# Kernel optimization log

Hardware: AMD Instinct MI355X
Metric: run time of the kernel (lower is better)

Reference implementation:

```python
import jax, jax.numpy as jnp
import numpy as np

T, P, E, H = 200000, 100000, 600000, 256

def setup_inputs() -> dict:
    key = jax.random.key(0)
    ks = jax.random.split(key, 8)
    x = jax.random.normal(ks[0], (T, H), dtype=jnp.float32)
    points = jax.random.normal(ks[1], (P, 3), dtype=jnp.float32)
    triangles = jax.random.randint(ks[2], (T, 3), 0, P)
    triangle_edges = jax.random.randint(ks[3], (2, E), 0, T)
    din = H + 9
    W1 = jax.random.normal(ks[4], (din, H), dtype=jnp.float32) / np.sqrt(din)
    b1 = jnp.zeros((H,), dtype=jnp.float32)
    W2 = jax.random.normal(ks[5], (H, H), dtype=jnp.float32) / np.sqrt(H)
    b2 = jnp.zeros((H,), dtype=jnp.float32)
    return {"x": x, "points": points, "triangles": triangles,
            "triangle_edges": triangle_edges, "W1": W1, "b1": b1, "W2": W2, "b2": b2}

def reference(x, points, triangles, triangle_edges, W1, b1, W2, b2):
    # Per-triangle geometry: [T, 3(corners), 3(xyz)]
    tp = points[triangles]
    e_ij = tp[:, 0] - tp[:, 1]
    e_ik = tp[:, 0] - tp[:, 2]
    e_jk = tp[:, 1] - tp[:, 2]
    edge_vectors = jnp.stack([e_ij, e_ik, e_jk], axis=1)  # [T,3,3]
    t_max = jnp.max(edge_vectors, axis=1).astype(x.dtype)  # [T,3]
    t_min = jnp.min(edge_vectors, axis=1).astype(x.dtype)  # [T,3]
    barycenters = jnp.mean(tp, axis=1).astype(x.dtype)     # [T,3]

    src = triangle_edges[0]
    tgt = triangle_edges[1]
    # Relative geometric descriptor per edge: [E, 9]
    r_n_k = jnp.concatenate([t_min[src] - t_min[tgt],
                             t_max[src] - t_max[tgt],
                             barycenters[src] - barycenters[tgt]], axis=1)
    feature_diff = x[src] - x[tgt]                          # [E, H]
    mlp_in = jnp.concatenate([r_n_k, feature_diff], axis=1)  # [E, H+9]
    h = jax.nn.relu(mlp_in @ W1 + b1)
    mlp_out = h @ W2 + b2                                   # [E, H]
    # Scatter-add back to source triangles (order-independent sum)
    new_features = jax.ops.segment_sum(mlp_out, src, num_segments=x.shape[0])
    return new_features.astype(x.dtype)
```

## Files before the change

### kernel.cpp

```cpp
#include <hip/hip_runtime.h>
#include <stdint.h>

typedef float f32x4v __attribute__((ext_vector_type(4)));
typedef short short8v __attribute__((ext_vector_type(8)));

__device__ __forceinline__ float bf2f(unsigned short u) {
  union { uint32_t i; float f; } v; v.i = ((uint32_t)u) << 16; return v.f;
}
__device__ __forceinline__ unsigned short f2bf(float f) {
  union { float f; uint32_t i; } v; v.f = f;
  uint32_t x = v.i;
  uint32_t r = (x + 0x7FFFu + ((x >> 16) & 1u)) >> 16;
  return (unsigned short)r;
}
__device__ __forceinline__ short8v cvt8(float4 a, float4 b) {
  short8v v;
  v[0] = (short)f2bf(a.x); v[1] = (short)f2bf(a.y);
  v[2] = (short)f2bf(a.z); v[3] = (short)f2bf(a.w);
  v[4] = (short)f2bf(b.x); v[5] = (short)f2bf(b.y);
  v[6] = (short)f2bf(b.z); v[7] = (short)f2bf(b.w);
  return v;
}

__global__ void zero_kernel(int* __restrict__ p, int n4) {
  int i = blockIdx.x * blockDim.x + threadIdx.x;
  int stride = gridDim.x * blockDim.x;
  for (; i < n4; i += stride) ((int4*)p)[i] = make_int4(0, 0, 0, 0);
}

__global__ void setup_kernel(const float* __restrict__ W1, const float* __restrict__ W2,
                             const float* __restrict__ points, const int* __restrict__ tri,
                             const int* __restrict__ te,
                             unsigned short* __restrict__ W1fT, unsigned short* __restrict__ W2T,
                             float* __restrict__ geo12, int* __restrict__ count,
                             int T, int E) {
  int i = blockIdx.x * blockDim.x + threadIdx.x;
  if (i < 256 * 288) {
    int n = i / 288, k = i % 288;
    float v = 0.f;
    if (k < 256) v = W1[(9 + k) * 256 + n];
    else if (k < 265) v = W1[(k - 256) * 256 + n];
    W1fT[i] = f2bf(v);
  }
  if (i < 256 * 256) {
    int n = i >> 8, k = i & 255;
    W2T[i] = f2bf(W2[k * 256 + n]);
  }
  if (i < T) {
    int t = i;
    int i0 = tri[3 * t], i1 = tri[3 * t + 1], i2 = tri[3 * t + 2];
    float g[12];
#pragma unroll
    for (int c = 0; c < 3; ++c) {
      float p0 = points[i0 * 3 + c], p1 = points[i1 * 3 + c], p2 = points[i2 * 3 + c];
      float e0 = p0 - p1, e1 = p0 - p2, e2 = p1 - p2;
      float mx = fmaxf(e0, fmaxf(e1, e2));
      float mn = fminf(e0, fminf(e1, e2));
      float bc = (p0 + p1 + p2) * (1.0f / 3.0f);
      g[c] = mn; g[3 + c] = mx; g[6 + c] = bc;
    }
    g[9] = 0.f; g[10] = 0.f; g[11] = 0.f;
    float4* o = (float4*)(geo12 + (size_t)t * 12);
    o[0] = make_float4(g[0], g[1], g[2], g[3]);
    o[1] = make_float4(g[4], g[5], g[6], g[7]);
    o[2] = make_float4(g[8], g[9], g[10], g[11]);
  }
  if (i < E) atomicAdd(&count[te[i]], 1);
}

__global__ void scan1_kernel(const int* __restrict__ count, int* __restrict__ incl,
                             int* __restrict__ blocksum, int T) {
  __shared__ int wsums[4];
  int tid = threadIdx.x, wave = tid >> 6, lane = tid & 63;
  int idx0 = blockIdx.x * 1024 + tid * 4;
  int c0 = 0, c1 = 0, c2 = 0, c3 = 0;
  if (idx0 + 3 < T) {
    int4 v = *(const int4*)(count + idx0);
    c0 = v.x; c1 = v.y; c2 = v.z; c3 = v.w;
  } else {
    if (idx0 < T) c0 = count[idx0];
    if (idx0 + 1 < T) c1 = count[idx0 + 1];
    if (idx0 + 2 < T) c2 = count[idx0 + 2];
  }
  int s = c0 + c1 + c2 + c3;
  int inclv = s;
#pragma unroll
  for (int off = 1; off < 64; off <<= 1) {
    int n = __shfl_up(inclv, off);
    if (lane >= off) inclv += n;
  }
  if (lane == 63) wsums[wave] = inclv;
  __syncthreads();
  int wbase = 0;
#pragma unroll
  for (int w = 0; w < 4; ++w) if (w < wave) wbase += wsums[w];
  int base = wbase + inclv - s;
  int e0 = base + c0, e1 = e0 + c1, e2 = e1 + c2, e3 = e2 + c3;
  if (idx0 < T) incl[idx0] = e0;
  if (idx0 + 1 < T) incl[idx0 + 1] = e1;
  if (idx0 + 2 < T) incl[idx0 + 2] = e2;
  if (idx0 + 3 < T) incl[idx0 + 3] = e3;
  if (tid == 255) blocksum[blockIdx.x] = wbase + inclv;
}

__global__ void scan2_kernel(const int* __restrict__ blocksum, int* __restrict__ blockbase, int nb) {
  __shared__ int wsums[4];
  int tid = threadIdx.x, wave = tid >> 6, lane = tid & 63;
  int v = (tid < nb) ? blocksum[tid] : 0;
  int inclv = v;
#pragma unroll
  for (int off = 1; off < 64; off <<= 1) {
    int n = __shfl_up(inclv, off);
    if (lane >= off) inclv += n;
  }
  if (lane == 63) wsums[wave] = inclv;
  __syncthreads();
  int wbase = 0;
#pragma unroll
  for (int w = 0; w < 4; ++w) if (w < wave) wbase += wsums[w];
  if (tid < nb) blockbase[tid] = wbase + inclv - v;
}

__global__ void scan3_kernel(const int* __restrict__ count, const int* __restrict__ incl,
                             const int* __restrict__ blockbase, int* __restrict__ offsets,
                             int* __restrict__ cursor, int T) {
  int idx = blockIdx.x * 1024 + threadIdx.x * 4;
  int bb = blockbase[blockIdx.x];
#pragma unroll
  for (int j = 0; j < 4; ++j) {
    int i = idx + j;
    if (i < T) {
      int o = incl[i] + bb;
      offsets[i + 1] = o;
      cursor[i] = o - count[i];
    }
  }
  if (blockIdx.x == 0 && threadIdx.x == 0) offsets[0] = 0;
}

__global__ void fill_kernel(const int* __restrict__ te, int* __restrict__ cursor,
                            int* __restrict__ tgt_list, int E) {
  int e = blockIdx.x * blockDim.x + threadIdx.x;
  if (e < E) {
    int s = te[e];
    int pos = atomicAdd(&cursor[s], 1);
    tgt_list[pos] = te[E + e];
  }
}

__launch_bounds__(1024, 4)
__global__ void ugemm_kernel(const float* __restrict__ x, const float* __restrict__ geo12,
                             const unsigned short* __restrict__ W1fT,
                             unsigned short* __restrict__ U, int T) {
  __shared__ alignas(16) unsigned short Bl[73728];
  int tid = threadIdx.x;
#pragma unroll
  for (int j = 0; j < 9; ++j) {
    int idx = tid + j * 1024;
    int n = idx / 36, c = idx % 36;
    int pc = (c < 32) ? (c ^ (n & 7)) : (32 + ((c - 32) ^ (n & 3)));
    short8v v = *(const short8v*)(W1fT + (size_t)n * 288 + c * 8);
    *(short8v*)(&Bl[n * 288 + pc * 8]) = v;
  }
  __syncthreads();
  int wid = tid >> 6, lane = tid & 63;
  int l15 = lane & 15, lhi = lane >> 4;
  int r7 = l15 & 7, r3 = l15 & 3;
  const unsigned short* lane_b = &Bl[l15 * 288];
  int strip = blockIdx.x * 16 + wid;
  if (strip * 16 >= T) return;
  int row = strip * 16 + l15;
  const float* xrow = x + (size_t)row * 256 + 8 * lhi;
  float4 ga = make_float4(0, 0, 0, 0), gb = make_float4(0, 0, 0, 0);
  if (lhi < 2) {
    const float* gp = geo12 + (size_t)row * 12 + lhi * 8;
    ga = *(const float4*)gp;
    gb = *(const float4*)(gp + 4);
  }
  float4 pa[4], pb[4];
#pragma unroll
  for (int k = 0; k < 4; ++k) {
    pa[k] = *(const float4*)(xrow + k * 32);
    pb[k] = *(const float4*)(xrow + k * 32 + 4);
  }
  f32x4v acc[16] = {};
#pragma unroll
  for (int kk = 0; kk < 8; ++kk) {
    float4 ca = pa[kk & 3], cb = pb[kk & 3];
    if (kk < 4) {
      pa[kk & 3] = *(const float4*)(xrow + (kk + 4) * 32);
      pb[kk & 3] = *(const float4*)(xrow + (kk + 4) * 32 + 4);
    }
    short8v av = cvt8(ca, cb);
    int pc = (kk * 4 + lhi) ^ r7;
    const unsigned short* bptr = lane_b + pc * 8;
#pragma unroll
    for (int nf = 0; nf < 16; ++nf) {
      short8v bv = *(const short8v*)(bptr + nf * 4608);
      acc[nf] = __builtin_amdgcn_mfma_f32_16x16x32_bf16(av, bv, acc[nf], 0, 0, 0);
    }
  }
  {
    short8v av = cvt8(ga, gb);
    int pc = 32 + (lhi ^ r3);
    const unsigned short* bptr = lane_b + pc * 8;
#pragma unroll
    for (int nf = 0; nf < 16; ++nf) {
      short8v bv = *(const short8v*)(bptr + nf * 4608);
      acc[nf] = __builtin_amdgcn_mfma_f32_16x16x32_bf16(av, bv, acc[nf], 0, 0, 0);
    }
  }
#pragma unroll
  for (int i = 0; i < 4; ++i) {
    int m = strip * 16 + 4 * lhi + i;
    unsigned short* urow = U + (size_t)m * 256 + l15;
#pragma unroll
    for (int nf = 0; nf < 16; ++nf)
      urow[nf * 16] = f2bf(acc[nf][i]);
  }
}

__launch_bounds__(256, 4)
__global__ void gather_kernel(const unsigned short* __restrict__ U,
                              const int* __restrict__ offsets,
                              const int* __restrict__ tgt_list,
                              const float* __restrict__ b1,
                              unsigned short* __restrict__ sum_h, int T) {
  int gid = blockIdx.x * blockDim.x + threadIdx.x;
  int half = (T + 1) >> 1;
  int pair = gid >> 5;
  if (pair >= half) return;
  int c8 = (gid & 31) * 8;
  int tA = pair, tB = pair + half;
  bool hasRowB = tB < T;
  int begA = offsets[tA], endA = offsets[tA + 1];
  int begB = hasRowB ? offsets[tB] : 0, endB = hasRowB ? offsets[tB + 1] : 0;
  float b1r[8];
  {
    float4 a = *(const float4*)(b1 + c8);
    float4 b = *(const float4*)(b1 + c8 + 4);
    b1r[0] = a.x; b1r[1] = a.y; b1r[2] = a.z; b1r[3] = a.w;
    b1r[4] = b.x; b1r[5] = b.y; b1r[6] = b.z; b1r[7] = b.w;
  }
  short8v uva = *(const short8v*)(U + (size_t)tA * 256 + c8);
  short8v uvb = *(const short8v*)(U + (size_t)(hasRowB ? tB : tA) * 256 + c8);
  float uA[8], sA[8], uB[8], sB[8];
#pragma unroll
  for (int j = 0; j < 8; ++j) {
    uA[j] = bf2f((unsigned short)uva[j]) + b1r[j]; sA[j] = 0.f;
    uB[j] = bf2f((unsigned short)uvb[j]) + b1r[j]; sB[j] = 0.f;
  }
  int eiA = begA, eiB = begB;
  while (eiA < endA || eiB < endB) {
    bool hasA = eiA < endA, hasB = eiB < endB;
    int laA = hasA ? endA - 1 : 0;
    int laB = hasB ? endB - 1 : 0;
    int a0 = hasA ? eiA : 0;
    int a1 = hasA ? min(eiA + 1, laA) : 0;
    int a2 = hasA ? min(eiA + 2, laA) : 0;
    int a3 = hasA ? min(eiA + 3, laA) : 0;
    int b0 = hasB ? eiB : 0;
    int b1i = hasB ? min(eiB + 1, laB) : 0;
    int b2i = hasB ? min(eiB + 2, laB) : 0;
    int b3 = hasB ? min(eiB + 3, laB) : 0;
    int gA0 = tgt_list[a0], gA1 = tgt_list[a1], gA2 = tgt_list[a2], gA3 = tgt_list[a3];
    int gB0 = tgt_list[b0], gB1 = tgt_list[b1i], gB2 = tgt_list[b2i], gB3 = tgt_list[b3];
    short8v vA0 = *(const short8v*)(U + (size_t)gA0 * 256 + c8);
    short8v vA1 = *(const short8v*)(U + (size_t)gA1 * 256 + c8);
    short8v vA2 = *(const short8v*)(U + (size_t)gA2 * 256 + c8);
    short8v vA3 = *(const short8v*)(U + (size_t)gA3 * 256 + c8);
    short8v vB0 = *(const short8v*)(U + (size_t)gB0 * 256 + c8);
    short8v vB1 = *(const short8v*)(U + (size_t)gB1 * 256 + c8);
    short8v vB2 = *(const short8v*)(U + (size_t)gB2 * 256 + c8);
    short8v vB3 = *(const short8v*)(U + (size_t)gB3 * 256 + c8);
    float mA0 = hasA ? 1.f : 0.f;
    float mA1 = (hasA && eiA + 1 <= laA) ? 1.f : 0.f;
    float mA2 = (hasA && eiA + 2 <= laA) ? 1.f : 0.f;
    float mA3 = (hasA && eiA + 3 <= laA) ? 1.f : 0.f;
    float mB0 = hasB ? 1.f : 0.f;
    float mB1 = (hasB && eiB + 1 <= laB) ? 1.f : 0.f;
    float mB2 = (hasB && eiB + 2 <= laB) ? 1.f : 0.f;
    float mB3 = (hasB && eiB + 3 <= laB) ? 1.f : 0.f;
#pragma unroll
    for (int j = 0; j < 8; ++j) {
      sA[j] += mA0 * fmaxf(uA[j] - bf2f((unsigned short)vA0[j]), 0.f)
             + mA1 * fmaxf(uA[j] - bf2f((unsigned short)vA1[j]), 0.f)
             + mA2 * fmaxf(uA[j] - bf2f((unsigned short)vA2[j]), 0.f)
             + mA3 * fmaxf(uA[j] - bf2f((unsigned short)vA3[j]), 0.f);
      sB[j] += mB0 * fmaxf(uB[j] - bf2f((unsigned short)vB0[j]), 0.f)
             + mB1 * fmaxf(uB[j] - bf2f((unsigned short)vB1[j]), 0.f)
             + mB2 * fmaxf(uB[j] - bf2f((unsigned short)vB2[j]), 0.f)
             + mB3 * fmaxf(uB[j] - bf2f((unsigned short)vB3[j]), 0.f);
    }
    if (hasA) eiA += 4;
    if (hasB) eiB += 4;
  }
  short8v hva, hvb;
#pragma unroll
  for (int j = 0; j < 8; ++j) { hva[j] = (short)f2bf(sA[j]); hvb[j] = (short)f2bf(sB[j]); }
  *(short8v*)(sum_h + (size_t)tA * 256 + c8) = hva;
  if (hasRowB) *(short8v*)(sum_h + (size_t)tB * 256 + c8) = hvb;
}

__launch_bounds__(1024, 4)
__global__ void out_gemm_kernel(const unsigned short* __restrict__ sum_h,
                                const unsigned short* __restrict__ W2T,
                                const int* __restrict__ count,
                                const float* __restrict__ b2,
                                float* __restrict__ out, int T) {
  __shared__ alignas(16) unsigned short Bl[65536];
  int tid = threadIdx.x;
#pragma unroll
  for (int j = 0; j < 8; ++j) {
    int idx = tid + j * 1024;
    int n = idx >> 5, c = idx & 31;
    int pc = c ^ (n & 7);
    short8v v = *(const short8v*)(W2T + (size_t)n * 256 + c * 8);
    *(short8v*)(&Bl[n * 256 + pc * 8]) = v;
  }
  __syncthreads();
  int wid = tid >> 6, lane = tid & 63;
  int l15 = lane & 15, lhi = lane >> 4;
  int r7 = l15 & 7;
  const unsigned short* lane_b = &Bl[l15 * 256];
  int strip = blockIdx.x * 16 + wid;
  if (strip * 16 >= T) return;
  int row = strip * 16 + l15;
  const unsigned short* arow = sum_h + (size_t)row * 256 + 8 * lhi;
  short8v pa[8];
#pragma unroll
  for (int k = 0; k < 8; ++k) pa[k] = *(const short8v*)(arow + k * 32);
  float b2r[16];
#pragma unroll
  for (int nf = 0; nf < 16; ++nf) b2r[nf] = b2[nf * 16 + l15];
  f32x4v acc[16] = {};
#pragma unroll
  for (int kk = 0; kk < 8; ++kk) {
    short8v av = pa[kk];
    int pc = (kk * 4 + lhi) ^ r7;
    const unsigned short* bptr = lane_b + pc * 8;
#pragma unroll
    for (int nf = 0; nf < 16; ++nf) {
      short8v bv = *(const short8v*)(bptr + nf * 4096);
      acc[nf] = __builtin_amdgcn_mfma_f32_16x16x32_bf16(av, bv, acc[nf], 0, 0, 0);
    }
  }
#pragma unroll
  for (int i = 0; i < 4; ++i) {
    int m = strip * 16 + 4 * lhi + i;
    float cnt = (float)count[m];
    float* orow = out + (size_t)m * 256 + l15;
#pragma unroll
    for (int nf = 0; nf < 16; ++nf)
      orow[nf * 16] = acc[nf][i] + cnt * b2r[nf];
  }
}

extern "C" void kernel_launch(void* const* d_in, const int* in_sizes, int n_in,
                              void* d_out, int out_size, void* d_ws, size_t ws_size,
                              hipStream_t stream) {
  const float* x = (const float*)d_in[0];
  const float* points = (const float*)d_in[1];
  const int* triangles = (const int*)d_in[2];
  const int* te = (const int*)d_in[3];
  const float* W1 = (const float*)d_in[4];
  const float* b1 = (const float*)d_in[5];
  const float* W2 = (const float*)d_in[6];
  const float* b2 = (const float*)d_in[7];
  float* out = (float*)d_out;
  int T = in_sizes[0] / 256;
  int E = in_sizes[3] / 2;

  char* ws = (char*)d_ws;
  size_t off = 0;
  auto alloc = [&](size_t bytes) {
    void* p = ws + off;
    off = (off + bytes + 255) & ~(size_t)255;
    return p;
  };
  unsigned short* U     = (unsigned short*)alloc((size_t)T * 256 * 2);
  float*          geo12 = (float*)alloc(((size_t)T * 12 + 16) * 4);
  unsigned short* W1fT  = (unsigned short*)alloc((size_t)256 * 288 * 2);
  unsigned short* W2T   = (unsigned short*)alloc((size_t)256 * 256 * 2);
  int* count   = (int*)alloc((size_t)(T + 4) * 4);
  int* offsets = (int*)alloc((size_t)(T + 1) * 4);
  int* cursor  = (int*)alloc((size_t)T * 4);
  int* tgtl    = (int*)alloc((size_t)E * 4);
  int* incl    = (int*)alloc((size_t)T * 4);
  int* bsum    = (int*)alloc(256 * 4);
  int* bbase   = (int*)alloc(256 * 4);
  unsigned short* sum_h = (unsigned short*)alloc((size_t)T * 256 * 2);
  if (off > ws_size) return;

  int nb1 = (T + 1023) / 1024;
  int nstrips = (T + 15) / 16;
  int ngemm = (nstrips + 15) / 16;
  zero_kernel<<<200, 256, 0, stream>>>(count, (T + 3) / 4);
  {
    int mx = max(E, max(T, 256 * 288));
    setup_kernel<<<(mx + 255) / 256, 256, 0, stream>>>(W1, W2, points, triangles, te,
                                                       W1fT, W2T, geo12, count, T, E);
  }
  scan1_kernel<<<nb1, 256, 0, stream>>>(count, incl, bsum, T);
  scan2_kernel<<<1, 256, 0, stream>>>(bsum, bbase, nb1);
  scan3_kernel<<<nb1, 256, 0, stream>>>(count, incl, bbase, offsets, cursor, T);
  fill_kernel<<<(E + 255) / 256, 256, 0, stream>>>(te, cursor, tgtl, E);
  ugemm_kernel<<<ngemm, 1024, 0, stream>>>(x, geo12, W1fT, U, T);
  {
    int half = (T + 1) >> 1;
    gather_kernel<<<(half * 32 + 255) / 256, 256, 0, stream>>>(U, offsets, tgtl, b1, sum_h, T);
  }
  out_gemm_kernel<<<ngemm, 1024, 0, stream>>>(sum_h, W2T, count, b2, out, T);
}
```

Before: 331.9 us.

## Retile GEMM waves to 32x128 tiles sharing B fragments across two row blocks

Both the U GEMM and the output GEMM now give each wave 32 rows by 128 columns instead of 16 rows by 256 columns, with two waves splitting N per strip. Each B fragment read from LDS feeds two MFMAs, which halves LDS traffic per MFMA. The A prefetch depth is cut from four slots to two to hold register pressure steady. The cost is that every x/sum_h row is now loaded by two waves, doubling global reads of A, which L2 is expected to absorb.

```diff
diff --git a/kernel.cpp b/kernel.cpp
--- a/kernel.cpp
+++ b/kernel.cpp
@@ -166,57 +166,75 @@
   int wid = tid >> 6, lane = tid & 63;
   int l15 = lane & 15, lhi = lane >> 4;
   int r7 = l15 & 7, r3 = l15 & 3;
-  const unsigned short* lane_b = &Bl[l15 * 288];
-  int strip = blockIdx.x * 16 + wid;
-  if (strip * 16 >= T) return;
-  int row = strip * 16 + l15;
-  const float* xrow = x + (size_t)row * 256 + 8 * lhi;
-  float4 ga = make_float4(0, 0, 0, 0), gb = make_float4(0, 0, 0, 0);
-  if (lhi < 2) {
-    const float* gp = geo12 + (size_t)row * 12 + lhi * 8;
-    ga = *(const float4*)gp;
-    gb = *(const float4*)(gp + 4);
-  }
-  float4 pa[4], pb[4];
-#pragma unroll
-  for (int k = 0; k < 4; ++k) {
-    pa[k] = *(const float4*)(xrow + k * 32);
-    pb[k] = *(const float4*)(xrow + k * 32 + 4);
-  }
-  f32x4v acc[16] = {};
+  int strip = blockIdx.x * 8 + (wid >> 1);
+  int nhalf = wid & 1;
+  const unsigned short* lane_b = &Bl[(nhalf * 128 + l15) * 288];
+  if (strip * 32 >= T) return;
+  int row0 = strip * 32 + l15;
+  int row1 = row0 + 16;
+  const float* xr0 = x + (size_t)row0 * 256 + 8 * lhi;
+  const float* xr1 = x + (size_t)row1 * 256 + 8 * lhi;
+  float4 pa0[2], pb0[2], pa1[2], pb1[2];
+#pragma unroll
+  for (int k = 0; k < 2; ++k) {
+    pa0[k] = *(const float4*)(xr0 + k * 32);
+    pb0[k] = *(const float4*)(xr0 + k * 32 + 4);
+    pa1[k] = *(const float4*)(xr1 + k * 32);
+    pb1[k] = *(const float4*)(xr1 + k * 32 + 4);
+  }
+  f32x4v acc[2][8] = {};
 #pragma unroll
   for (int kk = 0; kk < 8; ++kk) {
-    float4 ca = pa[kk & 3], cb = pb[kk & 3];
-    if (kk < 4) {
-      pa[kk & 3] = *(const float4*)(xrow + (kk + 4) * 32);
-      pb[kk & 3] = *(const float4*)(xrow + (kk + 4) * 32 + 4);
-    }
-    short8v av = cvt8(ca, cb);
+    int sl = kk & 1;
+    float4 ca0 = pa0[sl], cb0 = pb0[sl];
+    float4 ca1 = pa1[sl], cb1 = pb1[sl];
+    if (kk < 6) {
+      pa0[sl] = *(const float4*)(xr0 + (kk + 2) * 32);
+      pb0[sl] = *(const float4*)(xr0 + (kk + 2) * 32 + 4);
+      pa1[sl] = *(const float4*)(xr1 + (kk + 2) * 32);
+      pb1[sl] = *(const float4*)(xr1 + (kk + 2) * 32 + 4);
+    }
+    short8v av0 = cvt8(ca0, cb0);
+    short8v av1 = cvt8(ca1, cb1);
     int pc = (kk * 4 + lhi) ^ r7;
     const unsigned short* bptr = lane_b + pc * 8;
 #pragma unroll
-    for (int nf = 0; nf < 16; ++nf) {
+    for (int nf = 0; nf < 8; ++nf) {
       short8v bv = *(const short8v*)(bptr + nf * 4608);
-      acc[nf] = __builtin_amdgcn_mfma_f32_16x16x32_bf16(av, bv, acc[nf], 0, 0, 0);
+      acc[0][nf] = __builtin_amdgcn_mfma_f32_16x16x32_bf16(av0, bv, acc[0][nf], 0, 0, 0);
+      acc[1][nf] = __builtin_amdgcn_mfma_f32_16x16x32_bf16(av1, bv, acc[1][nf], 0, 0, 0);
     }
   }
   {
-    short8v av = cvt8(ga, gb);
+    float4 ga0 = make_float4(0, 0, 0, 0), gb0 = make_float4(0, 0, 0, 0);
+    float4 ga1 = make_float4(0, 0, 0, 0), gb1 = make_float4(0, 0, 0, 0);
+    if (lhi < 2) {
+      const float* gp0 = geo12 + (size_t)row0 * 12 + lhi * 8;
+      const float* gp1 = geo12 + (size_t)row1 * 12 + lhi * 8;
+      ga0 = *(const float4*)gp0; gb0 = *(const float4*)(gp0 + 4);
+      ga1 = *(const float4*)gp1; gb1 = *(const float4*)(gp1 + 4);
+    }
+    short8v av0 = cvt8(ga0, gb0);
+    short8v av1 = cvt8(ga1, gb1);
     int pc = 32 + (lhi ^ r3);
     const unsigned short* bptr = lane_b + pc * 8;
 #pragma unroll
-    for (int nf = 0; nf < 16; ++nf) {
+    for (int nf = 0; nf < 8; ++nf) {
       short8v bv = *(const short8v*)(bptr + nf * 4608);
-      acc[nf] = __builtin_amdgcn_mfma_f32_16x16x32_bf16(av, bv, acc[nf], 0, 0, 0);
-    }
-  }
-#pragma unroll
-  for (int i = 0; i < 4; ++i) {
-    int m = strip * 16 + 4 * lhi + i;
-    unsigned short* urow = U + (size_t)m * 256 + l15;
-#pragma unroll
-    for (int nf = 0; nf < 16; ++nf)
-      urow[nf * 16] = f2bf(acc[nf][i]);
+      acc[0][nf] = __builtin_amdgcn_mfma_f32_16x16x32_bf16(av0, bv, acc[0][nf], 0, 0, 0);
+      acc[1][nf] = __builtin_amdgcn_mfma_f32_16x16x32_bf16(av1, bv, acc[1][nf], 0, 0, 0);
+    }
+  }
+#pragma unroll
+  for (int mf = 0; mf < 2; ++mf) {
+#pragma unroll
+    for (int i = 0; i < 4; ++i) {
+      int m = strip * 32 + mf * 16 + 4 * lhi + i;
+      unsigned short* urow = U + (size_t)m * 256 + nhalf * 128 + l15;
+#pragma unroll
+      for (int nf = 0; nf < 8; ++nf)
+        urow[nf * 16] = f2bf(acc[mf][nf][i]);
+    }
   }
 }
 
@@ -322,37 +340,52 @@
   int wid = tid >> 6, lane = tid & 63;
   int l15 = lane & 15, lhi = lane >> 4;
   int r7 = l15 & 7;
-  const unsigned short* lane_b = &Bl[l15 * 256];
-  int strip = blockIdx.x * 16 + wid;
-  if (strip * 16 >= T) return;
-  int row = strip * 16 + l15;
-  const unsigned short* arow = sum_h + (size_t)row * 256 + 8 * lhi;
-  short8v pa[8];
-#pragma unroll
-  for (int k = 0; k < 8; ++k) pa[k] = *(const short8v*)(arow + k * 32);
-  float b2r[16];
-#pragma unroll
-  for (int nf = 0; nf < 16; ++nf) b2r[nf] = b2[nf * 16 + l15];
-  f32x4v acc[16] = {};
+  int strip = blockIdx.x * 8 + (wid >> 1);
+  int nhalf = wid & 1;
+  const unsigned short* lane_b = &Bl[(nhalf * 128 + l15) * 256];
+  if (strip * 32 >= T) return;
+  int row0 = strip * 32 + l15;
+  int row1 = row0 + 16;
+  const unsigned short* ar0 = sum_h + (size_t)row0 * 256 + 8 * lhi;
+  const unsigned short* ar1 = sum_h + (size_t)row1 * 256 + 8 * lhi;
+  short8v pa0[2], pa1[2];
+#pragma unroll
+  for (int k = 0; k < 2; ++k) {
+    pa0[k] = *(const short8v*)(ar0 + k * 32);
+    pa1[k] = *(const short8v*)(ar1 + k * 32);
+  }
+  float b2r[8];
+#pragma unroll
+  for (int nf = 0; nf < 8; ++nf) b2r[nf] = b2[nhalf * 128 + nf * 16 + l15];
+  f32x4v acc[2][8] = {};
 #pragma unroll
   for (int kk = 0; kk < 8; ++kk) {
-    short8v av = pa[kk];
+    int sl = kk & 1;
+    short8v av0 = pa0[sl], av1 = pa1[sl];
+    if (kk < 6) {
+      pa0[sl] = *(const short8v*)(ar0 + (kk + 2) * 32);
+      pa1[sl] = *(const short8v*)(ar1 + (kk + 2) * 32);
+    }
     int pc = (kk * 4 + lhi) ^ r7;
     const unsigned short* bptr = lane_b + pc * 8;
 #pragma unroll
-    for (int nf = 0; nf < 16; ++nf) {
+    for (int nf = 0; nf < 8; ++nf) {
       short8v bv = *(const short8v*)(bptr + nf * 4096);
-      acc[nf] = __builtin_amdgcn_mfma_f32_16x16x32_bf16(av, bv, acc[nf], 0, 0, 0);
-    }
-  }
-#pragma unroll
-  for (int i = 0; i < 4; ++i) {
-    int m = strip * 16 + 4 * lhi + i;
-    float cnt = (float)count[m];
-    float* orow = out + (size_t)m * 256 + l15;
-#pragma unroll
-    for (int nf = 0; nf < 16; ++nf)
-      orow[nf * 16] = acc[nf][i] + cnt * b2r[nf];
+      acc[0][nf] = __builtin_amdgcn_mfma_f32_16x16x32_bf16(av0, bv, acc[0][nf], 0, 0, 0);
+      acc[1][nf] = __builtin_amdgcn_mfma_f32_16x16x32_bf16(av1, bv, acc[1][nf], 0, 0, 0);
+    }
+  }
+#pragma unroll
+  for (int mf = 0; mf < 2; ++mf) {
+#pragma unroll
+    for (int i = 0; i < 4; ++i) {
+      int m = strip * 32 + mf * 16 + 4 * lhi + i;
+      float cnt = (float)count[m];
+      float* orow = out + (size_t)m * 256 + nhalf * 128 + l15;
+#pragma unroll
+      for (int nf = 0; nf < 8; ++nf)
+        orow[nf * 16] = acc[mf][nf][i] + cnt * b2r[nf];
+    }
   }
 }
 
@@ -393,8 +426,8 @@
   if (off > ws_size) return;
 
   int nb1 = (T + 1023) / 1024;
-  int nstrips = (T + 15) / 16;
-  int ngemm = (nstrips + 15) / 16;
+  int nstrips32 = (T + 31) / 32;
+  int ngemm = (nstrips32 + 7) / 8;
   zero_kernel<<<200, 256, 0, stream>>>(count, (T + 3) / 4);
   {
     int mx = max(E, max(T, 256 * 288));
```

Measured after the change: 343.9 us. 3.6% more time.

## Fuse three-pass prefix scan into single-pass decoupled look-back scan

Applied to the files above, without the earlier changes.

Replaces the three scan kernels (block scan, block-sum scan, fixup) with one kernel that uses a ticket counter for in-order block IDs and decoupled look-back across blocks. The status, aggregate and inclusive arrays are placed right after the count buffer, so the existing zero kernel clears them. This removes two kernel launches and the intermediate round trip through global memory. In exchange it adds serial spin-waiting on predecessor blocks through atomics, and the look-back is done by a single thread per block.

```diff
diff --git a/kernel.cpp b/kernel.cpp
--- a/kernel.cpp
+++ b/kernel.cpp
@@ -68,11 +68,18 @@
   if (i < E) atomicAdd(&count[te[i]], 1);
 }
 
-__global__ void scan1_kernel(const int* __restrict__ count, int* __restrict__ incl,
-                             int* __restrict__ blocksum, int T) {
+__global__ void scan_fused_kernel(const int* __restrict__ count, int* __restrict__ offsets,
+                                  int* __restrict__ cursor, int* __restrict__ status,
+                                  int* __restrict__ aggv, int* __restrict__ inclv,
+                                  int* __restrict__ ticket, int T) {
   __shared__ int wsums[4];
+  __shared__ int sbid;
+  __shared__ int sexcl;
   int tid = threadIdx.x, wave = tid >> 6, lane = tid & 63;
-  int idx0 = blockIdx.x * 1024 + tid * 4;
+  if (tid == 0) sbid = atomicAdd(ticket, 1);
+  __syncthreads();
+  int bid = sbid;
+  int idx0 = bid * 1024 + tid * 4;
   int c0 = 0, c1 = 0, c2 = 0, c3 = 0;
   if (idx0 + 3 < T) {
     int4 v = *(const int4*)(count + idx0);
@@ -83,59 +90,46 @@
     if (idx0 + 2 < T) c2 = count[idx0 + 2];
   }
   int s = c0 + c1 + c2 + c3;
-  int inclv = s;
+  int inclx = s;
 #pragma unroll
   for (int off = 1; off < 64; off <<= 1) {
-    int n = __shfl_up(inclv, off);
-    if (lane >= off) inclv += n;
-  }
-  if (lane == 63) wsums[wave] = inclv;
+    int n = __shfl_up(inclx, off);
+    if (lane >= off) inclx += n;
+  }
+  if (lane == 63) wsums[wave] = inclx;
   __syncthreads();
   int wbase = 0;
 #pragma unroll
   for (int w = 0; w < 4; ++w) if (w < wave) wbase += wsums[w];
-  int base = wbase + inclv - s;
-  int e0 = base + c0, e1 = e0 + c1, e2 = e1 + c2, e3 = e2 + c3;
-  if (idx0 < T) incl[idx0] = e0;
-  if (idx0 + 1 < T) incl[idx0 + 1] = e1;
-  if (idx0 + 2 < T) incl[idx0 + 2] = e2;
-  if (idx0 + 3 < T) incl[idx0 + 3] = e3;
-  if (tid == 255) blocksum[blockIdx.x] = wbase + inclv;
-}
-
-__global__ void scan2_kernel(const int* __restrict__ blocksum, int* __restrict__ blockbase, int nb) {
-  __shared__ int wsums[4];
-  int tid = threadIdx.x, wave = tid >> 6, lane = tid & 63;
-  int v = (tid < nb) ? blocksum[tid] : 0;
-  int inclv = v;
-#pragma unroll
-  for (int off = 1; off < 64; off <<= 1) {
-    int n = __shfl_up(inclv, off);
-    if (lane >= off) inclv += n;
-  }
-  if (lane == 63) wsums[wave] = inclv;
+  int total = wsums[0] + wsums[1] + wsums[2] + wsums[3];
+  if (tid == 0) {
+    aggv[bid] = total;
+    __threadfence();
+    atomicExch(&status[bid], 1);
+  }
+  if (tid == 0) {
+    int excl = 0;
+    int j = bid - 1;
+    while (j >= 0) {
+      int st;
+      do { st = atomicAdd(&status[j], 0); } while (st == 0);
+      if (st == 2) { excl += atomicAdd(&inclv[j], 0); break; }
+      excl += atomicAdd(&aggv[j], 0);
+      --j;
+    }
+    inclv[bid] = excl + total;
+    __threadfence();
+    atomicExch(&status[bid], 2);
+    sexcl = excl;
+  }
   __syncthreads();
-  int wbase = 0;
-#pragma unroll
-  for (int w = 0; w < 4; ++w) if (w < wave) wbase += wsums[w];
-  if (tid < nb) blockbase[tid] = wbase + inclv - v;
-}
-
-__global__ void scan3_kernel(const int* __restrict__ count, const int* __restrict__ incl,
-                             const int* __restrict__ blockbase, int* __restrict__ offsets,
-                             int* __restrict__ cursor, int T) {
-  int idx = blockIdx.x * 1024 + threadIdx.x * 4;
-  int bb = blockbase[blockIdx.x];
-#pragma unroll
-  for (int j = 0; j < 4; ++j) {
-    int i = idx + j;
-    if (i < T) {
-      int o = incl[i] + bb;
-      offsets[i + 1] = o;
-      cursor[i] = o - count[i];
-    }
-  }
-  if (blockIdx.x == 0 && threadIdx.x == 0) offsets[0] = 0;
+  int base = sexcl + wbase + inclx - s;
+  int r = base;
+  if (idx0 < T)     { cursor[idx0] = r;     r += c0; offsets[idx0 + 1] = r; }
+  if (idx0 + 1 < T) { cursor[idx0 + 1] = r; r += c1; offsets[idx0 + 2] = r; }
+  if (idx0 + 2 < T) { cursor[idx0 + 2] = r; r += c2; offsets[idx0 + 3] = r; }
+  if (idx0 + 3 < T) { cursor[idx0 + 3] = r; r += c3; offsets[idx0 + 4] = r; }
+  if (bid == 0 && tid == 0) offsets[0] = 0;
 }
 
 __global__ void fill_kernel(const int* __restrict__ te, int* __restrict__ cursor,
@@ -382,28 +376,29 @@
   float*          geo12 = (float*)alloc(((size_t)T * 12 + 16) * 4);
   unsigned short* W1fT  = (unsigned short*)alloc((size_t)256 * 288 * 2);
   unsigned short* W2T   = (unsigned short*)alloc((size_t)256 * 256 * 2);
-  int* count   = (int*)alloc((size_t)(T + 4) * 4);
+  int nb1 = (T + 1023) / 1024;
+  int* count   = (int*)alloc((size_t)(T + 4) * 4 + (size_t)(3 * nb1 + 8) * 4);
+  int* status  = count + T + 4;
+  int* aggv    = status + nb1;
+  int* inclv   = aggv + nb1;
+  int* ticket  = inclv + nb1;
+  int zero_ints = T + 4 + 3 * nb1 + 8;
   int* offsets = (int*)alloc((size_t)(T + 1) * 4);
   int* cursor  = (int*)alloc((size_t)T * 4);
   int* tgtl    = (int*)alloc((size_t)E * 4);
-  int* incl    = (int*)alloc((size_t)T * 4);
-  int* bsum    = (int*)alloc(256 * 4);
-  int* bbase   = (int*)alloc(256 * 4);
   unsigned short* sum_h = (unsigned short*)alloc((size_t)T * 256 * 2);
   if (off > ws_size) return;
 
-  int nb1 = (T + 1023) / 1024;
   int nstrips = (T + 15) / 16;
   int ngemm = (nstrips + 15) / 16;
-  zero_kernel<<<200, 256, 0, stream>>>(count, (T + 3) / 4);
+  zero_kernel<<<200, 256, 0, stream>>>(count, (zero_ints + 3) / 4);
   {
     int mx = max(E, max(T, 256 * 288));
     setup_kernel<<<(mx + 255) / 256, 256, 0, stream>>>(W1, W2, points, triangles, te,
                                                        W1fT, W2T, geo12, count, T, E);
   }
-  scan1_kernel<<<nb1, 256, 0, stream>>>(count, incl, bsum, T);
-  scan2_kernel<<<1, 256, 0, stream>>>(bsum, bbase, nb1);
-  scan3_kernel<<<nb1, 256, 0, stream>>>(count, incl, bbase, offsets, cursor, T);
+  scan_fused_kernel<<<nb1, 256, 0, stream>>>(count, offsets, cursor, status, aggv, inclv,
+                                             ticket, T);
   fill_kernel<<<(E + 255) / 256, 256, 0, stream>>>(te, cursor, tgtl, E);
   ugemm_kernel<<<ngemm, 1024, 0, stream>>>(x, geo12, W1fT, U, T);
   {
```

Measured after the change: 349.5 us. 5.3% more time.
